# Kernel tuning notes

Hardware: AMD Instinct MI355X
Metric: run time of the kernel (lower is better)

Reference implementation:

```python
import jax, jax.numpy as jnp
import numpy as np


def conv2d(x, w, b=None, pad=0):
    # x: [N,C,H,W], w: [O,I,kh,kw] (cross-correlation, matches torch conv2d)
    out = jax.lax.conv_general_dilated(
        x, w, window_strides=(1, 1), padding=[(pad, pad), (pad, pad)],
        dimension_numbers=('NCHW', 'OIHW', 'NCHW'))
    if b is not None:
        out = out + b[None, :, None, None]
    return out


def se_block(f, w1, b1, w2, b2):
    # squeeze-excite: global avg pool -> 1x1 conv -> relu -> 1x1 conv -> sigmoid
    s = jnp.mean(f, axis=(2, 3), keepdims=True)
    s = jax.nn.relu(conv2d(s, w1, b1, pad=0))
    s = jax.nn.sigmoid(conv2d(s, w2, b2, pad=0))
    return f * s


def setup_inputs() -> dict:
    key = jax.random.key(0)
    ks = jax.random.split(key, 32)
    B, C, H, W = 8, 3, 128, 128
    F_, S, K = 128, 8, 72  # features, squeeze, n basis kernels
    rn = lambda k, shp, sc=0.05: (jax.random.normal(k, shp, dtype=jnp.float32) * sc)
    return {
        'x': jax.random.normal(ks[0], (B, C, H, W), dtype=jnp.float32),
        'w_head': rn(ks[1], (F_, C, 3, 3)), 'b_head': rn(ks[2], (F_,)),
        'w_h1a': rn(ks[3], (F_, F_, 3, 3)), 'b_h1a': rn(ks[4], (F_,)),
        'w_h1b': rn(ks[5], (F_, F_, 3, 3)), 'b_h1b': rn(ks[6], (F_,)),
        'du1_w1': rn(ks[7], (S, F_, 1, 1)), 'du1_b1': rn(ks[8], (S,)),
        'du1_w2': rn(ks[9], (F_, S, 1, 1)), 'du1_b2': rn(ks[10], (F_,)),
        'w_h2a': rn(ks[11], (F_, F_, 3, 3)), 'b_h2a': rn(ks[12], (F_,)),
        'w_h2b': rn(ks[13], (F_, F_, 3, 3)), 'b_h2b': rn(ks[14], (F_,)),
        'du2_w1': rn(ks[15], (S, F_, 1, 1)), 'du2_b1': rn(ks[16], (S,)),
        'du2_w2': rn(ks[17], (F_, S, 1, 1)), 'du2_b2': rn(ks[18], (F_,)),
        'w_tail': rn(ks[19], (K, F_, 3, 3)), 'b_tail': rn(ks[20], (K,)),
        'kernel': rn(ks[21], (K, 1, 5, 5), 0.2),  # fixed 72x5x5 basis
    }


def reference(x, w_head, b_head, w_h1a, b_h1a, w_h1b, b_h1b,
              du1_w1, du1_b1, du1_w2, du1_b2,
              w_h2a, b_h2a, w_h2b, b_h2b,
              du2_w1, du2_b1, du2_w2, du2_b2,
              w_tail, b_tail, kernel):
    B, C, H, W = x.shape
    K = kernel.shape[0]
    # trunk: head -> (conv relu)x2 -> SE -> (conv relu)x2 -> SE -> tail
    f = conv2d(x, w_head, b_head, pad=1)
    f = jax.nn.relu(conv2d(f, w_h1a, b_h1a, pad=1))
    f = jax.nn.relu(conv2d(f, w_h1b, b_h1b, pad=1))
    f = se_block(f, du1_w1, du1_b1, du1_w2, du1_b2)
    f = jax.nn.relu(conv2d(f, w_h2a, b_h2a, pad=1))
    f = jax.nn.relu(conv2d(f, w_h2b, b_h2b, pad=1))
    f = se_block(f, du2_w1, du2_b1, du2_w2, du2_b2)
    wgt = conv2d(f, w_tail, b_tail, pad=1).reshape(B, 1, K, H, W)
    # dynamic filtering: apply 72 fixed 5x5 basis kernels per channel, then
    # per-pixel weighted sum over the 72 basis responses
    xp = jnp.pad(x, ((0, 0), (0, 0), (2, 2), (2, 2)), mode='reflect')
    xp = xp.reshape(B * C, 1, H + 4, W + 4)
    x_com = conv2d(xp, kernel, None, pad=0).reshape(B, C, K, H, W)
    out = jnp.sum(wgt * x_com, axis=2)  # [B,3,H,W]
    return out
```

## Files before the change

kernel.cpp:

```cpp
#include <hip/hip_runtime.h>
#include <math.h>


typedef __attribute__((ext_vector_type(8))) short bf16x8;
typedef __attribute__((ext_vector_type(4))) float f32x4;

__device__ inline float bf2f(unsigned short u) {
    unsigned v = ((unsigned)u) << 16;
    return __builtin_bit_cast(float, v);
}
__device__ inline unsigned short f2bf(float f) {
    unsigned u = __builtin_bit_cast(unsigned, f);
    u += 0x7FFF + ((u >> 16) & 1);
    return (unsigned short)(u >> 16);
}

__global__ __launch_bounds__(256) void head_conv(
    const float* __restrict__ x, const float* __restrict__ w,
    const float* __restrict__ bias, unsigned short* __restrict__ out)
{
    __shared__ float wlds[216];
    __shared__ float tile[3][34 * 34];
    const int tid = threadIdx.x, cog = blockIdx.y, b = blockIdx.z;
    const int tile_y = (blockIdx.x >> 2) * 32, tile_x = (blockIdx.x & 3) * 32;

    if (tid < 216) {
        int co = tid & 7, rest = tid >> 3, tap = rest % 9, ci = rest / 9;
        wlds[tid] = w[((cog * 8 + co) * 3 + ci) * 9 + tap];
    }
    for (int idx = tid; idx < 3 * 34 * 34; idx += 256) {
        int ci = idx / 1156, rem = idx - ci * 1156;
        int r = rem / 34, c = rem - r * 34;
        int gy = tile_y - 1 + r, gx = tile_x - 1 + c;
        float v = 0.f;
        if ((unsigned)gy < 128u && (unsigned)gx < 128u)
            v = x[(((size_t)(b * 3 + ci)) << 14) + (gy << 7) + gx];
        tile[ci][rem] = v;
    }
    __syncthreads();

    const int ty = tid >> 4, tx = tid & 15, py = ty * 2;
    float acc[2][2][8];
    #pragma unroll
    for (int r = 0; r < 2; ++r)
        #pragma unroll
        for (int h = 0; h < 2; ++h)
            #pragma unroll
            for (int co = 0; co < 8; ++co) acc[r][h][co] = 0.f;

    #pragma unroll
    for (int ci = 0; ci < 3; ++ci) {
        #pragma unroll
        for (int ky = 0; ky < 3; ++ky) {
            #pragma unroll
            for (int kx = 0; kx < 3; ++kx) {
                const float* wp = wlds + (ci * 9 + ky * 3 + kx) * 8;
                float i00 = tile[ci][(py + ky) * 34 + tx + kx];
                float i01 = tile[ci][(py + ky) * 34 + tx + 16 + kx];
                float i10 = tile[ci][(py + 1 + ky) * 34 + tx + kx];
                float i11 = tile[ci][(py + 1 + ky) * 34 + tx + 16 + kx];
                #pragma unroll
                for (int co = 0; co < 8; ++co) {
                    float wv = wp[co];
                    acc[0][0][co] += i00 * wv;
                    acc[0][1][co] += i01 * wv;
                    acc[1][0][co] += i10 * wv;
                    acc[1][1][co] += i11 * wv;
                }
            }
        }
    }

    #pragma unroll
    for (int r = 0; r < 2; ++r) {
        #pragma unroll
        for (int h = 0; h < 2; ++h) {
            int gy = tile_y + py + r, gx = tile_x + tx + h * 16;
            bf16x8 pv;
            #pragma unroll
            for (int co = 0; co < 8; ++co)
                pv[co] = (short)f2bf(acc[r][h][co] + bias[cog * 8 + co]);
            *(bf16x8*)(out + (((((size_t)b << 14) + gy * 128 + gx)) << 7) + cog * 8) = pv;
        }
    }
}

template <int LM, int NTW, int WNSPLIT, int DOMEAN, int TAILFUSE>
__global__ __launch_bounds__(256, 2) void conv_mfma(
    const unsigned short* __restrict__ in, const unsigned short* __restrict__ wT,
    size_t wstride, const float* __restrict__ bias, unsigned short* __restrict__ out,
    float* __restrict__ meanb, const float* __restrict__ x,
    const unsigned short* __restrict__ kb, float* __restrict__ outf,
    int Coutp, int Cout, int relu)
{
    __shared__ unsigned short lds[TAILFUSE ? 26624 : 20736];
    const int tid = threadIdx.x;
    const int b = blockIdx.y;
    const int row0 = (blockIdx.x >> 3) << 4;
    const int col0 = (blockIdx.x & 7) << 4;
    const int l = tid & 63, wv = tid >> 6;
    const int li = l & 15, lq = l >> 4;
    const int m_base = WNSPLIT ? (wv >> 1) * LM : wv * LM;
    const int n_base = WNSPLIT ? (wv & 1) * NTW : 0;
    const size_t inb = ((size_t)b) << 14;
    const unsigned short* wbase = wT + (size_t)b * wstride;

    f32x4 acc[LM][NTW];
    #pragma unroll
    for (int lm = 0; lm < LM; ++lm)
        #pragma unroll
        for (int nt = 0; nt < NTW; ++nt)
            acc[lm][nt] = (f32x4){0.f, 0.f, 0.f, 0.f};

    #pragma unroll 1
    for (int half = 0; half < 2; ++half) {
        __syncthreads();
        for (int u = tid; u < 2592; u += 256) {
            int px = u >> 3, g = u & 7;
            int hr = px / 18, hc = px - hr * 18;
            int gy = row0 - 1 + hr, gx = col0 - 1 + hc;
            bf16x8 v = {0, 0, 0, 0, 0, 0, 0, 0};
            if ((unsigned)gy < 128u && (unsigned)gx < 128u)
                v = *(const bf16x8*)(in + ((inb + (gy << 7) + gx) << 7) + half * 64 + g * 8);
            int p = g ^ (px & 7);
            *(bf16x8*)(lds + px * 64 + p * 8) = v;
        }
        __syncthreads();

        auto loadB = [&](bf16x8 (&dst)[NTW], int s) {
            int tap = s >> 1, kcl = s & 1;
            const unsigned short* p = wbase +
                (size_t)(tap * 4 + half * 2 + kcl) * (Coutp * 32) +
                (n_base * 16 + li) * 32 + lq * 8;
            #pragma unroll
            for (int nt = 0; nt < NTW; ++nt)
                dst[nt] = *(const bf16x8*)(p + nt * 512);
        };
        auto compute = [&](bf16x8 (&bf)[NTW], int s) {
            int tap = s >> 1, kcl = s & 1;
            int ky = tap / 3, kx = tap - ky * 3;
            int g = kcl * 4 + lq;
            #pragma unroll
            for (int lm = 0; lm < LM; ++lm) {
                int px = (m_base + lm + ky) * 18 + li + kx;
                bf16x8 af = *(const bf16x8*)(lds + px * 64 + ((g ^ (px & 7)) * 8));
                #pragma unroll
                for (int nt = 0; nt < NTW; ++nt)
                    acc[lm][nt] = __builtin_amdgcn_mfma_f32_16x16x32_bf16(
                        af, bf[nt], acc[lm][nt], 0, 0, 0);
            }
        };

        bf16x8 bufA[NTW], bufB[NTW];
        loadB(bufA, 0);
        #pragma unroll 1
        for (int it = 0; it < 18; it += 2) {
            loadB(bufB, it + 1);
            compute(bufA, it);
            if (it + 2 < 18) loadB(bufA, it + 2);
            compute(bufB, it + 1);
        }
    }

    float bv[NTW], msum[NTW];
    #pragma unroll
    for (int nt = 0; nt < NTW; ++nt) {
        int co = (n_base + nt) * 16 + li;
        bv[nt] = (co < Cout) ? bias[co] : 0.f;
        msum[nt] = 0.f;
    }

    if (TAILFUSE) {
        __syncthreads();
        #pragma unroll
        for (int lm = 0; lm < LM; ++lm) {
            int rowl = m_base + lm;
            #pragma unroll
            for (int r = 0; r < 4; ++r) {
                int coll = lq * 4 + r;
                #pragma unroll
                for (int nt = 0; nt < NTW; ++nt)
                    lds[(rowl * 16 + coll) * 104 + nt * 16 + li] =
                        f2bf(acc[lm][nt][r] + bv[nt]);
            }
        }
        {
            bf16x8 z = {0, 0, 0, 0, 0, 0, 0, 0};
            *(bf16x8*)(lds + tid * 104 + 80) = z;
            *(bf16x8*)(lds + tid * 104 + 88) = z;
        }
        __syncthreads();

        f32x4 eacc[4][2];
        #pragma unroll
        for (int mm = 0; mm < 4; ++mm)
            #pragma unroll
            for (int nt = 0; nt < 2; ++nt)
                eacc[mm][nt] = (f32x4){0.f, 0.f, 0.f, 0.f};
        #pragma unroll
        for (int s = 0; s < 3; ++s) {
            bf16x8 kbf[2];
            #pragma unroll
            for (int nt = 0; nt < 2; ++nt)
                kbf[nt] = *(const bf16x8*)(kb + ((s * 2 + nt) * 16 + li) * 32 + lq * 8);
            #pragma unroll
            for (int mm = 0; mm < 4; ++mm) {
                int px = (wv * 4 + mm) * 16 + li;
                bf16x8 pf = *(const bf16x8*)(lds + px * 104 + s * 32 + lq * 8);
                #pragma unroll
                for (int nt = 0; nt < 2; ++nt)
                    eacc[mm][nt] = __builtin_amdgcn_mfma_f32_16x16x32_bf16(
                        pf, kbf[nt], eacc[mm][nt], 0, 0, 0);
            }
        }
        __syncthreads();

        float* elds = (float*)lds;
        #pragma unroll
        for (int mm = 0; mm < 4; ++mm) {
            #pragma unroll
            for (int nt = 0; nt < 2; ++nt) {
                int i = nt * 16 + li;
                if (i < 25) {
                    #pragma unroll
                    for (int r = 0; r < 4; ++r) {
                        int px = (wv * 4 + mm) * 16 + lq * 4 + r;
                        elds[px * 33 + i] = eacc[mm][nt][r];
                    }
                }
            }
        }
        __syncthreads();

        const int h = row0 + (tid >> 4), w = col0 + (tid & 15);
        const int pix = h * 128 + w;
        float e[25];
        #pragma unroll
        for (int i = 0; i < 25; ++i) e[i] = elds[tid * 33 + i];

        int yy[5], xx[5];
        #pragma unroll
        for (int d = 0; d < 5; ++d) {
            int y = h - 2 + d;
            yy[d] = y < 0 ? -y : (y > 127 ? 254 - y : y);
            int xv = w - 2 + d;
            xx[d] = xv < 0 ? -xv : (xv > 127 ? 254 - xv : xv);
        }
        #pragma unroll
        for (int c = 0; c < 3; ++c) {
            const float* xc = x + ((size_t)(b * 3 + c) << 14);
            float s = 0.f;
            #pragma unroll
            for (int dy = 0; dy < 5; ++dy)
                #pragma unroll
                for (int dx = 0; dx < 5; ++dx)
                    s += e[dy * 5 + dx] * xc[yy[dy] * 128 + xx[dx]];
            outf[((size_t)(b * 3 + c) << 14) + pix] = s;
        }
        return;
    }

    #pragma unroll
    for (int lm = 0; lm < LM; ++lm) {
        int row = row0 + m_base + lm;
        #pragma unroll
        for (int r = 0; r < 4; ++r) {
            int col = col0 + lq * 4 + r;
            size_t pbase = (inb + row * 128 + col) * (size_t)Coutp;
            #pragma unroll
            for (int nt = 0; nt < NTW; ++nt) {
                float v = acc[lm][nt][r] + bv[nt];
                if (relu) v = fmaxf(v, 0.f);
                if (DOMEAN) msum[nt] += v;
                out[pbase + (n_base + nt) * 16 + li] = f2bf(v);
            }
        }
    }
    if (DOMEAN) {
        #pragma unroll
        for (int nt = 0; nt < NTW; ++nt) {
            float t = msum[nt];
            t += __shfl_xor(t, 16, 64);
            t += __shfl_xor(t, 32, 64);
            if (lq == 0)
                atomicAdd(&meanb[b * 128 + (n_base + nt) * 16 + li], t);
        }
    }
}

__device__ inline void wtrans_one(const float* w, unsigned short* wT,
                                  int Co, int Coutp, int idx)
{
    int ch = idx & 31;
    int rest = idx >> 5;
    int co = rest % Coutp;
    int slice = rest / Coutp;
    int kc = slice & 3, tap = slice >> 2;
    float v = (co < Co) ? w[((size_t)(co * 128 + kc * 32 + ch)) * 9 + tap] : 0.f;
    wT[idx] = f2bf(v);
}

__global__ __launch_bounds__(256) void wtrans6(
    const float* __restrict__ w0, const float* __restrict__ w1,
    const float* __restrict__ w2, const float* __restrict__ w3,
    const float* __restrict__ w4, const float* __restrict__ kern,
    unsigned short* __restrict__ t0, unsigned short* __restrict__ t1,
    unsigned short* __restrict__ t2, unsigned short* __restrict__ t3,
    unsigned short* __restrict__ t4, unsigned short* __restrict__ kb,
    float* __restrict__ meanz)
{
    int idx = blockIdx.x * 256 + threadIdx.x;
    int y = blockIdx.y;
    if (y < 4) {
        const float* w = y == 0 ? w0 : y == 1 ? w1 : y == 2 ? w2 : w3;
        unsigned short* t = y == 0 ? t0 : y == 1 ? t1 : y == 2 ? t2 : t3;
        wtrans_one(w, t, 128, 128, idx);
    } else if (y == 4) {
        if (idx < 9 * 4 * 80 * 32) wtrans_one(w4, t4, 72, 80, idx);
    } else {
        if (idx < 3072) {
            int lq = (idx & 31) >> 3, j = idx & 7;
            int row = idx >> 5;
            int li = row & 15, snt = row >> 4;
            int s = snt >> 1, nt = snt & 1;
            int co = s * 32 + lq * 8 + j, i = nt * 16 + li;
            float v = (co < 72 && i < 25) ? kern[co * 25 + i] : 0.f;
            kb[idx] = f2bf(v);
        }
        if (idx < 2048) meanz[idx] = 0.f;
    }
}

__global__ __launch_bounds__(256) void wscale8f(
    const unsigned short* __restrict__ wT, const float* __restrict__ meanb,
    const float* __restrict__ w1, const float* __restrict__ b1,
    const float* __restrict__ w2, const float* __restrict__ b2,
    unsigned short* __restrict__ out, int Coutp)
{
    const int b = blockIdx.y, c = threadIdx.x;
    __shared__ float h1[8];
    __shared__ float sl[128];
    if (c < 8) {
        float s = 0.f;
        for (int j = 0; j < 128; ++j) s += w1[c * 128 + j] * meanb[b * 128 + j];
        h1[c] = fmaxf(s * (1.f / 16384.f) + b1[c], 0.f);
    }
    __syncthreads();
    if (c < 128) {
        float s = b2[c];
        #pragma unroll
        for (int j = 0; j < 8; ++j) s += w2[c * 8 + j] * h1[j];
        sl[c] = 1.f / (1.f + expf(-s));
    }
    __syncthreads();
    int r = blockIdx.x * 256 + c;
    int ch = r & 31;
    int kc = ((r >> 5) / Coutp) & 3;
    out[(size_t)b * (9 * 4 * Coutp * 32) + r] = f2bf(bf2f(wT[r]) * sl[kc * 32 + ch]);
}

extern "C" void kernel_launch(void* const* d_in, const int* in_sizes, int n_in,
                              void* d_out, int out_size, void* d_ws, size_t ws_size,
                              hipStream_t stream)
{
    const float* x      = (const float*)d_in[0];
    const float* w_head = (const float*)d_in[1];
    const float* b_head = (const float*)d_in[2];
    const float* w_h1a  = (const float*)d_in[3];
    const float* b_h1a  = (const float*)d_in[4];
    const float* w_h1b  = (const float*)d_in[5];
    const float* b_h1b  = (const float*)d_in[6];
    const float* du1_w1 = (const float*)d_in[7];
    const float* du1_b1 = (const float*)d_in[8];
    const float* du1_w2 = (const float*)d_in[9];
    const float* du1_b2 = (const float*)d_in[10];
    const float* w_h2a  = (const float*)d_in[11];
    const float* b_h2a  = (const float*)d_in[12];
    const float* w_h2b  = (const float*)d_in[13];
    const float* b_h2b  = (const float*)d_in[14];
    const float* du2_w1 = (const float*)d_in[15];
    const float* du2_b1 = (const float*)d_in[16];
    const float* du2_w2 = (const float*)d_in[17];
    const float* du2_b2 = (const float*)d_in[18];
    const float* w_tail = (const float*)d_in[19];
    const float* b_tail = (const float*)d_in[20];
    const float* kern   = (const float*)d_in[21];
    float* out = (float*)d_out;

    unsigned short* fb0  = (unsigned short*)d_ws;
    unsigned short* fb1  = fb0 + 16777216;
    unsigned short* wt1  = fb1 + 16777216;
    unsigned short* wt2  = wt1 + 147456;
    unsigned short* wt3  = wt2 + 147456;
    unsigned short* wt4  = wt3 + 147456;
    unsigned short* wtt  = wt4 + 147456;
    unsigned short* wsa  = wtt + 92160;
    unsigned short* wst  = wsa + 8 * 147456;
    unsigned short* kbb  = wst + 8 * 92160;
    float* mean1  = (float*)(kbb + 3072);
    float* mean2  = mean1 + 1024;

    dim3 blk(256);
    wtrans6<<<dim3(576, 6), blk, 0, stream>>>(w_h1a, w_h1b, w_h2a, w_h2b, w_tail,
                                              kern, wt1, wt2, wt3, wt4, wtt, kbb,
                                              mean1);

    head_conv<<<dim3(16, 16, 8), blk, 0, stream>>>(x, w_head, b_head, fb0);

    dim3 cgrid(64, 8);
    conv_mfma<8, 4, 1, 0, 0><<<cgrid, blk, 0, stream>>>(
        fb0, wt1, 0, b_h1a, fb1, nullptr, nullptr, nullptr, nullptr, 128, 128, 1);
    conv_mfma<8, 4, 1, 1, 0><<<cgrid, blk, 0, stream>>>(
        fb1, wt2, 0, b_h1b, fb0, mean1, nullptr, nullptr, nullptr, 128, 128, 1);

    wscale8f<<<dim3(576, 8), blk, 0, stream>>>(wt3, mean1, du1_w1, du1_b1,
                                               du1_w2, du1_b2, wsa, 128);

    conv_mfma<8, 4, 1, 0, 0><<<cgrid, blk, 0, stream>>>(
        fb0, wsa, 147456, b_h2a, fb1, nullptr, nullptr, nullptr, nullptr, 128, 128, 1);
    conv_mfma<8, 4, 1, 1, 0><<<cgrid, blk, 0, stream>>>(
        fb1, wt4, 0, b_h2b, fb0, mean2, nullptr, nullptr, nullptr, 128, 128, 1);

    wscale8f<<<dim3(360, 8), blk, 0, stream>>>(wtt, mean2, du2_w1, du2_b1,
                                               du2_w2, du2_b2, wst, 80);

    conv_mfma<4, 5, 0, 0, 1><<<cgrid, blk, 0, stream>>>(
        fb0, wst, 92160, b_tail, nullptr, nullptr, x, kbb, out, 80, 72, 0);
}
```

Measured before the change: 335.0 us.

## Prefetch second input-channel half into registers during first-half MFMA compute

The 3x3 conv kernel loaded both 64-channel halves of the input halo tile into LDS sequentially, stalling on global loads before each half. It now issues the global loads for the second half into 11 registers per thread while the first half's MFMA loop runs, then writes them to LDS after a barrier. This hides global-load latency behind compute, but adds about 44 VGPRs per thread, which may lower occupancy or cause spills.

```diff
diff --git a/kernel.cpp b/kernel.cpp
--- a/kernel.cpp
+++ b/kernel.cpp
@@ -112,54 +112,90 @@
         for (int nt = 0; nt < NTW; ++nt)
             acc[lm][nt] = (f32x4){0.f, 0.f, 0.f, 0.f};
 
-    #pragma unroll 1
-    for (int half = 0; half < 2; ++half) {
-        __syncthreads();
-        for (int u = tid; u < 2592; u += 256) {
+    auto loadB = [&](int half, bf16x8 (&dst)[NTW], int s) {
+        int tap = s >> 1, kcl = s & 1;
+        const unsigned short* p = wbase +
+            (size_t)(tap * 4 + half * 2 + kcl) * (Coutp * 32) +
+            (n_base * 16 + li) * 32 + lq * 8;
+        #pragma unroll
+        for (int nt = 0; nt < NTW; ++nt)
+            dst[nt] = *(const bf16x8*)(p + nt * 512);
+    };
+    auto compute = [&](bf16x8 (&bf)[NTW], int s) {
+        int tap = s >> 1, kcl = s & 1;
+        int ky = tap / 3, kx = tap - ky * 3;
+        int g = kcl * 4 + lq;
+        #pragma unroll
+        for (int lm = 0; lm < LM; ++lm) {
+            int px = (m_base + lm + ky) * 18 + li + kx;
+            bf16x8 af = *(const bf16x8*)(lds + px * 64 + ((g ^ (px & 7)) * 8));
+            #pragma unroll
+            for (int nt = 0; nt < NTW; ++nt)
+                acc[lm][nt] = __builtin_amdgcn_mfma_f32_16x16x32_bf16(
+                    af, bf[nt], acc[lm][nt], 0, 0, 0);
+        }
+    };
+
+    #pragma unroll
+    for (int k = 0; k < 11; ++k) {
+        int u = tid + (k << 8);
+        if (u < 2592) {
             int px = u >> 3, g = u & 7;
             int hr = px / 18, hc = px - hr * 18;
             int gy = row0 - 1 + hr, gx = col0 - 1 + hc;
             bf16x8 v = {0, 0, 0, 0, 0, 0, 0, 0};
             if ((unsigned)gy < 128u && (unsigned)gx < 128u)
-                v = *(const bf16x8*)(in + ((inb + (gy << 7) + gx) << 7) + half * 64 + g * 8);
-            int p = g ^ (px & 7);
-            *(bf16x8*)(lds + px * 64 + p * 8) = v;
-        }
-        __syncthreads();
-
-        auto loadB = [&](bf16x8 (&dst)[NTW], int s) {
-            int tap = s >> 1, kcl = s & 1;
-            const unsigned short* p = wbase +
-                (size_t)(tap * 4 + half * 2 + kcl) * (Coutp * 32) +
-                (n_base * 16 + li) * 32 + lq * 8;
-            #pragma unroll
-            for (int nt = 0; nt < NTW; ++nt)
-                dst[nt] = *(const bf16x8*)(p + nt * 512);
-        };
-        auto compute = [&](bf16x8 (&bf)[NTW], int s) {
-            int tap = s >> 1, kcl = s & 1;
-            int ky = tap / 3, kx = tap - ky * 3;
-            int g = kcl * 4 + lq;
-            #pragma unroll
-            for (int lm = 0; lm < LM; ++lm) {
-                int px = (m_base + lm + ky) * 18 + li + kx;
-                bf16x8 af = *(const bf16x8*)(lds + px * 64 + ((g ^ (px & 7)) * 8));
-                #pragma unroll
-                for (int nt = 0; nt < NTW; ++nt)
-                    acc[lm][nt] = __builtin_amdgcn_mfma_f32_16x16x32_bf16(
-                        af, bf[nt], acc[lm][nt], 0, 0, 0);
-            }
-        };
-
-        bf16x8 bufA[NTW], bufB[NTW];
-        loadB(bufA, 0);
-        #pragma unroll 1
-        for (int it = 0; it < 18; it += 2) {
-            loadB(bufB, it + 1);
-            compute(bufA, it);
-            if (it + 2 < 18) loadB(bufA, it + 2);
-            compute(bufB, it + 1);
-        }
+                v = *(const bf16x8*)(in + ((inb + (gy << 7) + gx) << 7) + g * 8);
+            *(bf16x8*)(lds + px * 64 + ((g ^ (px & 7)) * 8)) = v;
+        }
+    }
+    __syncthreads();
+
+    bf16x8 bufA[NTW], bufB[NTW];
+    bf16x8 sreg[11];
+    loadB(0, bufA, 0);
+    loadB(0, bufB, 1);
+    #pragma unroll
+    for (int k = 0; k < 11; ++k) {
+        int u = tid + (k << 8);
+        sreg[k] = (bf16x8){0, 0, 0, 0, 0, 0, 0, 0};
+        if (u < 2592) {
+            int px = u >> 3, g = u & 7;
+            int hr = px / 18, hc = px - hr * 18;
+            int gy = row0 - 1 + hr, gx = col0 - 1 + hc;
+            if ((unsigned)gy < 128u && (unsigned)gx < 128u)
+                sreg[k] = *(const bf16x8*)(in + ((inb + (gy << 7) + gx) << 7) + 64 + g * 8);
+        }
+    }
+    compute(bufA, 0);
+    loadB(0, bufA, 2);
+    compute(bufB, 1);
+    #pragma unroll 1
+    for (int it = 2; it < 18; it += 2) {
+        loadB(0, bufB, it + 1);
+        compute(bufA, it);
+        if (it + 2 < 18) loadB(0, bufA, it + 2);
+        compute(bufB, it + 1);
+    }
+
+    __syncthreads();
+    #pragma unroll
+    for (int k = 0; k < 11; ++k) {
+        int u = tid + (k << 8);
+        if (u < 2592) {
+            int px = u >> 3, g = u & 7;
+            *(bf16x8*)(lds + px * 64 + ((g ^ (px & 7)) * 8)) = sreg[k];
+        }
+    }
+    __syncthreads();
+
+    loadB(1, bufA, 0);
+    #pragma unroll 1
+    for (int it = 0; it < 18; it += 2) {
+        loadB(1, bufB, it + 1);
+        compute(bufA, it);
+        if (it + 2 < 18) loadB(1, bufA, it + 2);
+        compute(bufB, it + 1);
     }
 
     float bv[NTW], msum[NTW];
```

Result: slower. 343.4 us (+2.5%).

## Double-buffer input halo in quarters via direct global-to-LDS async loads

Applied to the files above, without the earlier changes.

Replaces the two-half synchronous register-staged LDS fill with four 32-channel quarters loaded directly into LDS using global_load_lds, double-buffered so the next quarter's halo load overlaps MFMA compute on the current one. Out-of-bounds pixels read from a zeroed workspace buffer instead of branching to a zero store, and precomputed per-thread source offsets replace the per-iteration division. This removes the exposed load-then-sync bubble per half at the cost of more barriers, a new swizzle scheme, and reliance on the zero buffer being cleared by the setup kernel.

```diff
diff --git a/kernel.cpp b/kernel.cpp
--- a/kernel.cpp
+++ b/kernel.cpp
@@ -91,7 +91,7 @@
     size_t wstride, const float* __restrict__ bias, unsigned short* __restrict__ out,
     float* __restrict__ meanb, const float* __restrict__ x,
     const unsigned short* __restrict__ kb, float* __restrict__ outf,
-    int Coutp, int Cout, int relu)
+    const unsigned short* __restrict__ zbuf, int Coutp, int Cout, int relu)
 {
     __shared__ unsigned short lds[TAILFUSE ? 26624 : 20736];
     const int tid = threadIdx.x;
@@ -102,7 +102,7 @@
     const int li = l & 15, lq = l >> 4;
     const int m_base = WNSPLIT ? (wv >> 1) * LM : wv * LM;
     const int n_base = WNSPLIT ? (wv & 1) * NTW : 0;
-    const size_t inb = ((size_t)b) << 14;
+    const unsigned short* inb7 = in + ((size_t)b << 21);
     const unsigned short* wbase = wT + (size_t)b * wstride;
 
     f32x4 acc[LM][NTW];
@@ -112,54 +112,79 @@
         for (int nt = 0; nt < NTW; ++nt)
             acc[lm][nt] = (f32x4){0.f, 0.f, 0.f, 0.f};
 
-    #pragma unroll 1
-    for (int half = 0; half < 2; ++half) {
-        __syncthreads();
-        for (int u = tid; u < 2592; u += 256) {
-            int px = u >> 3, g = u & 7;
-            int hr = px / 18, hc = px - hr * 18;
-            int gy = row0 - 1 + hr, gx = col0 - 1 + hc;
-            bf16x8 v = {0, 0, 0, 0, 0, 0, 0, 0};
-            if ((unsigned)gy < 128u && (unsigned)gx < 128u)
-                v = *(const bf16x8*)(in + ((inb + (gy << 7) + gx) << 7) + half * 64 + g * 8);
-            int p = g ^ (px & 7);
-            *(bf16x8*)(lds + px * 64 + p * 8) = v;
-        }
-        __syncthreads();
-
-        auto loadB = [&](bf16x8 (&dst)[NTW], int s) {
-            int tap = s >> 1, kcl = s & 1;
-            const unsigned short* p = wbase +
-                (size_t)(tap * 4 + half * 2 + kcl) * (Coutp * 32) +
-                (n_base * 16 + li) * 32 + lq * 8;
+    int soff[6];
+    #pragma unroll
+    for (int i = 0; i < 6; ++i) {
+        int base = (i < 5) ? (i * 4 + wv) * 64 : 1232;
+        int u = base + l;
+        int px = u >> 2, p = u & 3;
+        int g = p ^ (px & 3);
+        int hr = px / 18, hc = px - hr * 18;
+        int gy = row0 - 1 + hr, gx = col0 - 1 + hc;
+        soff[i] = ((unsigned)gy < 128u && (unsigned)gx < 128u)
+                      ? ((((gy << 7) + gx) << 7) + g * 8) : -1;
+    }
+
+    auto stageQ = [&](int q) {
+        unsigned short* dbuf = lds + (q & 1) * 10368;
+        const int qo = q * 32;
+        #pragma unroll
+        for (int i = 0; i < 6; ++i) {
+            if (i == 5 && wv != 0) continue;
+            int base = (i < 5) ? (i * 4 + wv) * 64 : 1232;
+            const unsigned short* src =
+                (soff[i] >= 0) ? (inb7 + soff[i] + qo) : zbuf;
+            __builtin_amdgcn_global_load_lds((const void*)src,
+                                             (void*)(dbuf + base * 8), 16, 0, 0);
+        }
+    };
+    auto loadB = [&](int q, bf16x8 (&dst)[NTW], int tap) {
+        const unsigned short* p = wbase +
+            (size_t)(tap * 4 + q) * (Coutp * 32) +
+            (n_base * 16 + li) * 32 + lq * 8;
+        #pragma unroll
+        for (int nt = 0; nt < NTW; ++nt)
+            dst[nt] = *(const bf16x8*)(p + nt * 512);
+    };
+    auto compute = [&](const unsigned short* lbuf, bf16x8 (&bf)[NTW], int tap) {
+        int ky = tap / 3, kx = tap - ky * 3;
+        #pragma unroll
+        for (int lm = 0; lm < LM; ++lm) {
+            int px = (m_base + lm + ky) * 18 + li + kx;
+            bf16x8 af = *(const bf16x8*)(lbuf + px * 32 + ((lq ^ (px & 3)) * 8));
             #pragma unroll
             for (int nt = 0; nt < NTW; ++nt)
-                dst[nt] = *(const bf16x8*)(p + nt * 512);
-        };
-        auto compute = [&](bf16x8 (&bf)[NTW], int s) {
-            int tap = s >> 1, kcl = s & 1;
-            int ky = tap / 3, kx = tap - ky * 3;
-            int g = kcl * 4 + lq;
-            #pragma unroll
-            for (int lm = 0; lm < LM; ++lm) {
-                int px = (m_base + lm + ky) * 18 + li + kx;
-                bf16x8 af = *(const bf16x8*)(lds + px * 64 + ((g ^ (px & 7)) * 8));
-                #pragma unroll
-                for (int nt = 0; nt < NTW; ++nt)
-                    acc[lm][nt] = __builtin_amdgcn_mfma_f32_16x16x32_bf16(
-                        af, bf[nt], acc[lm][nt], 0, 0, 0);
-            }
-        };
-
-        bf16x8 bufA[NTW], bufB[NTW];
-        loadB(bufA, 0);
-        #pragma unroll 1
-        for (int it = 0; it < 18; it += 2) {
-            loadB(bufB, it + 1);
-            compute(bufA, it);
-            if (it + 2 < 18) loadB(bufA, it + 2);
-            compute(bufB, it + 1);
-        }
+                acc[lm][nt] = __builtin_amdgcn_mfma_f32_16x16x32_bf16(
+                    af, bf[nt], acc[lm][nt], 0, 0, 0);
+        }
+    };
+
+    stageQ(0);
+    __syncthreads();
+    #pragma unroll
+    for (int q = 0; q < 4; ++q) {
+        const unsigned short* lbuf = lds + (q & 1) * 10368;
+        bf16x8 bA[NTW], bB[NTW];
+        loadB(q, bA, 0);
+        loadB(q, bB, 1);
+        if (q < 3) stageQ(q + 1);
+        compute(lbuf, bA, 0);
+        loadB(q, bA, 2);
+        compute(lbuf, bB, 1);
+        loadB(q, bB, 3);
+        compute(lbuf, bA, 2);
+        loadB(q, bA, 4);
+        compute(lbuf, bB, 3);
+        loadB(q, bB, 5);
+        compute(lbuf, bA, 4);
+        loadB(q, bA, 6);
+        compute(lbuf, bB, 5);
+        loadB(q, bB, 7);
+        compute(lbuf, bA, 6);
+        loadB(q, bA, 8);
+        compute(lbuf, bB, 7);
+        compute(lbuf, bA, 8);
+        if (q < 3) __syncthreads();
     }
 
     float bv[NTW], msum[NTW];
@@ -266,7 +291,7 @@
         #pragma unroll
         for (int r = 0; r < 4; ++r) {
             int col = col0 + lq * 4 + r;
-            size_t pbase = (inb + row * 128 + col) * (size_t)Coutp;
+            size_t pbase = ((((size_t)b << 14) + row * 128 + col)) * (size_t)Coutp;
             #pragma unroll
             for (int nt = 0; nt < NTW; ++nt) {
                 float v = acc[lm][nt][r] + bv[nt];
@@ -327,7 +352,7 @@
             float v = (co < 72 && i < 25) ? kern[co * 25 + i] : 0.f;
             kb[idx] = f2bf(v);
         }
-        if (idx < 2048) meanz[idx] = 0.f;
+        if (idx < 2112) meanz[idx] = 0.f;
     }
 }
 
@@ -399,6 +424,7 @@
     unsigned short* kbb  = wst + 8 * 92160;
     float* mean1  = (float*)(kbb + 3072);
     float* mean2  = mean1 + 1024;
+    unsigned short* zbuf = (unsigned short*)(mean2 + 1024);
 
     dim3 blk(256);
     wtrans6<<<dim3(576, 6), blk, 0, stream>>>(w_h1a, w_h1b, w_h2a, w_h2b, w_tail,
@@ -409,21 +435,21 @@
 
     dim3 cgrid(64, 8);
     conv_mfma<8, 4, 1, 0, 0><<<cgrid, blk, 0, stream>>>(
-        fb0, wt1, 0, b_h1a, fb1, nullptr, nullptr, nullptr, nullptr, 128, 128, 1);
+        fb0, wt1, 0, b_h1a, fb1, nullptr, nullptr, nullptr, nullptr, zbuf, 128, 128, 1);
     conv_mfma<8, 4, 1, 1, 0><<<cgrid, blk, 0, stream>>>(
-        fb1, wt2, 0, b_h1b, fb0, mean1, nullptr, nullptr, nullptr, 128, 128, 1);
+        fb1, wt2, 0, b_h1b, fb0, mean1, nullptr, nullptr, nullptr, zbuf, 128, 128, 1);
 
     wscale8f<<<dim3(576, 8), blk, 0, stream>>>(wt3, mean1, du1_w1, du1_b1,
                                                du1_w2, du1_b2, wsa, 128);
 
     conv_mfma<8, 4, 1, 0, 0><<<cgrid, blk, 0, stream>>>(
-        fb0, wsa, 147456, b_h2a, fb1, nullptr, nullptr, nullptr, nullptr, 128, 128, 1);
+        fb0, wsa, 147456, b_h2a, fb1, nullptr, nullptr, nullptr, nullptr, zbuf, 128, 128, 1);
     conv_mfma<8, 4, 1, 1, 0><<<cgrid, blk, 0, stream>>>(
-        fb1, wt4, 0, b_h2b, fb0, mean2, nullptr, nullptr, nullptr, 128, 128, 1);
+        fb1, wt4, 0, b_h2b, fb0, mean2, nullptr, nullptr, nullptr, zbuf, 128, 128, 1);
 
     wscale8f<<<dim3(360, 8), blk, 0, stream>>>(wtt, mean2, du2_w1, du2_b1,
                                                du2_w2, du2_b2, wst, 80);
 
     conv_mfma<4, 5, 0, 0, 1><<<cgrid, blk, 0, stream>>>(
-        fb0, wst, 92160, b_tail, nullptr, nullptr, x, kbb, out, 80, 72, 0);
-}
+        fb0, wst, 92160, b_tail, nullptr, nullptr, x, kbb, out, zbuf, 80, 72, 0);
+}
```

Result: slower. 369.2 us (+10.2%).

## Fuse SE scaling into consumer convs and merge head conv with weight prep

Applied to the files above, without the earlier changes.

Removes the two wscale8f kernels that wrote per-batch scaled weight copies. Instead, each consuming conv computes the squeeze-excite scale from the accumulated means into LDS and, judging by the SCALEA template flag, applies it to the input activations it loads. It also merges the head conv and weight transposition into one prep kernel, cutting two launches and the per-batch weight traffic. In exchange, every conv block recomputes the small SE MLP and does an extra multiply on its staged activations.

```diff
diff --git a/kernel.cpp b/kernel.cpp
--- a/kernel.cpp
+++ b/kernel.cpp
@@ -13,279 +13,6 @@
     unsigned u = __builtin_bit_cast(unsigned, f);
     u += 0x7FFF + ((u >> 16) & 1);
     return (unsigned short)(u >> 16);
-}
-
-__global__ __launch_bounds__(256) void head_conv(
-    const float* __restrict__ x, const float* __restrict__ w,
-    const float* __restrict__ bias, unsigned short* __restrict__ out)
-{
-    __shared__ float wlds[216];
-    __shared__ float tile[3][34 * 34];
-    const int tid = threadIdx.x, cog = blockIdx.y, b = blockIdx.z;
-    const int tile_y = (blockIdx.x >> 2) * 32, tile_x = (blockIdx.x & 3) * 32;
-
-    if (tid < 216) {
-        int co = tid & 7, rest = tid >> 3, tap = rest % 9, ci = rest / 9;
-        wlds[tid] = w[((cog * 8 + co) * 3 + ci) * 9 + tap];
-    }
-    for (int idx = tid; idx < 3 * 34 * 34; idx += 256) {
-        int ci = idx / 1156, rem = idx - ci * 1156;
-        int r = rem / 34, c = rem - r * 34;
-        int gy = tile_y - 1 + r, gx = tile_x - 1 + c;
-        float v = 0.f;
-        if ((unsigned)gy < 128u && (unsigned)gx < 128u)
-            v = x[(((size_t)(b * 3 + ci)) << 14) + (gy << 7) + gx];
-        tile[ci][rem] = v;
-    }
-    __syncthreads();
-
-    const int ty = tid >> 4, tx = tid & 15, py = ty * 2;
-    float acc[2][2][8];
-    #pragma unroll
-    for (int r = 0; r < 2; ++r)
-        #pragma unroll
-        for (int h = 0; h < 2; ++h)
-            #pragma unroll
-            for (int co = 0; co < 8; ++co) acc[r][h][co] = 0.f;
-
-    #pragma unroll
-    for (int ci = 0; ci < 3; ++ci) {
-        #pragma unroll
-        for (int ky = 0; ky < 3; ++ky) {
-            #pragma unroll
-            for (int kx = 0; kx < 3; ++kx) {
-                const float* wp = wlds + (ci * 9 + ky * 3 + kx) * 8;
-                float i00 = tile[ci][(py + ky) * 34 + tx + kx];
-                float i01 = tile[ci][(py + ky) * 34 + tx + 16 + kx];
-                float i10 = tile[ci][(py + 1 + ky) * 34 + tx + kx];
-                float i11 = tile[ci][(py + 1 + ky) * 34 + tx + 16 + kx];
-                #pragma unroll
-                for (int co = 0; co < 8; ++co) {
-                    float wv = wp[co];
-                    acc[0][0][co] += i00 * wv;
-                    acc[0][1][co] += i01 * wv;
-                    acc[1][0][co] += i10 * wv;
-                    acc[1][1][co] += i11 * wv;
-                }
-            }
-        }
-    }
-
-    #pragma unroll
-    for (int r = 0; r < 2; ++r) {
-        #pragma unroll
-        for (int h = 0; h < 2; ++h) {
-            int gy = tile_y + py + r, gx = tile_x + tx + h * 16;
-            bf16x8 pv;
-            #pragma unroll
-            for (int co = 0; co < 8; ++co)
-                pv[co] = (short)f2bf(acc[r][h][co] + bias[cog * 8 + co]);
-            *(bf16x8*)(out + (((((size_t)b << 14) + gy * 128 + gx)) << 7) + cog * 8) = pv;
-        }
-    }
-}
-
-template <int LM, int NTW, int WNSPLIT, int DOMEAN, int TAILFUSE>
-__global__ __launch_bounds__(256, 2) void conv_mfma(
-    const unsigned short* __restrict__ in, const unsigned short* __restrict__ wT,
-    size_t wstride, const float* __restrict__ bias, unsigned short* __restrict__ out,
-    float* __restrict__ meanb, const float* __restrict__ x,
-    const unsigned short* __restrict__ kb, float* __restrict__ outf,
-    int Coutp, int Cout, int relu)
-{
-    __shared__ unsigned short lds[TAILFUSE ? 26624 : 20736];
-    const int tid = threadIdx.x;
-    const int b = blockIdx.y;
-    const int row0 = (blockIdx.x >> 3) << 4;
-    const int col0 = (blockIdx.x & 7) << 4;
-    const int l = tid & 63, wv = tid >> 6;
-    const int li = l & 15, lq = l >> 4;
-    const int m_base = WNSPLIT ? (wv >> 1) * LM : wv * LM;
-    const int n_base = WNSPLIT ? (wv & 1) * NTW : 0;
-    const size_t inb = ((size_t)b) << 14;
-    const unsigned short* wbase = wT + (size_t)b * wstride;
-
-    f32x4 acc[LM][NTW];
-    #pragma unroll
-    for (int lm = 0; lm < LM; ++lm)
-        #pragma unroll
-        for (int nt = 0; nt < NTW; ++nt)
-            acc[lm][nt] = (f32x4){0.f, 0.f, 0.f, 0.f};
-
-    #pragma unroll 1
-    for (int half = 0; half < 2; ++half) {
-        __syncthreads();
-        for (int u = tid; u < 2592; u += 256) {
-            int px = u >> 3, g = u & 7;
-            int hr = px / 18, hc = px - hr * 18;
-            int gy = row0 - 1 + hr, gx = col0 - 1 + hc;
-            bf16x8 v = {0, 0, 0, 0, 0, 0, 0, 0};
-            if ((unsigned)gy < 128u && (unsigned)gx < 128u)
-                v = *(const bf16x8*)(in + ((inb + (gy << 7) + gx) << 7) + half * 64 + g * 8);
-            int p = g ^ (px & 7);
-            *(bf16x8*)(lds + px * 64 + p * 8) = v;
-        }
-        __syncthreads();
-
-        auto loadB = [&](bf16x8 (&dst)[NTW], int s) {
-            int tap = s >> 1, kcl = s & 1;
-            const unsigned short* p = wbase +
-                (size_t)(tap * 4 + half * 2 + kcl) * (Coutp * 32) +
-                (n_base * 16 + li) * 32 + lq * 8;
-            #pragma unroll
-            for (int nt = 0; nt < NTW; ++nt)
-                dst[nt] = *(const bf16x8*)(p + nt * 512);
-        };
-        auto compute = [&](bf16x8 (&bf)[NTW], int s) {
-            int tap = s >> 1, kcl = s & 1;
-            int ky = tap / 3, kx = tap - ky * 3;
-            int g = kcl * 4 + lq;
-            #pragma unroll
-            for (int lm = 0; lm < LM; ++lm) {
-                int px = (m_base + lm + ky) * 18 + li + kx;
-                bf16x8 af = *(const bf16x8*)(lds + px * 64 + ((g ^ (px & 7)) * 8));
-                #pragma unroll
-                for (int nt = 0; nt < NTW; ++nt)
-                    acc[lm][nt] = __builtin_amdgcn_mfma_f32_16x16x32_bf16(
-                        af, bf[nt], acc[lm][nt], 0, 0, 0);
-            }
-        };
-
-        bf16x8 bufA[NTW], bufB[NTW];
-        loadB(bufA, 0);
-        #pragma unroll 1
-        for (int it = 0; it < 18; it += 2) {
-            loadB(bufB, it + 1);
-            compute(bufA, it);
-            if (it + 2 < 18) loadB(bufA, it + 2);
-            compute(bufB, it + 1);
-        }
-    }
-
-    float bv[NTW], msum[NTW];
-    #pragma unroll
-    for (int nt = 0; nt < NTW; ++nt) {
-        int co = (n_base + nt) * 16 + li;
-        bv[nt] = (co < Cout) ? bias[co] : 0.f;
-        msum[nt] = 0.f;
-    }
-
-    if (TAILFUSE) {
-        __syncthreads();
-        #pragma unroll
-        for (int lm = 0; lm < LM; ++lm) {
-            int rowl = m_base + lm;
-            #pragma unroll
-            for (int r = 0; r < 4; ++r) {
-                int coll = lq * 4 + r;
-                #pragma unroll
-                for (int nt = 0; nt < NTW; ++nt)
-                    lds[(rowl * 16 + coll) * 104 + nt * 16 + li] =
-                        f2bf(acc[lm][nt][r] + bv[nt]);
-            }
-        }
-        {
-            bf16x8 z = {0, 0, 0, 0, 0, 0, 0, 0};
-            *(bf16x8*)(lds + tid * 104 + 80) = z;
-            *(bf16x8*)(lds + tid * 104 + 88) = z;
-        }
-        __syncthreads();
-
-        f32x4 eacc[4][2];
-        #pragma unroll
-        for (int mm = 0; mm < 4; ++mm)
-            #pragma unroll
-            for (int nt = 0; nt < 2; ++nt)
-                eacc[mm][nt] = (f32x4){0.f, 0.f, 0.f, 0.f};
-        #pragma unroll
-        for (int s = 0; s < 3; ++s) {
-            bf16x8 kbf[2];
-            #pragma unroll
-            for (int nt = 0; nt < 2; ++nt)
-                kbf[nt] = *(const bf16x8*)(kb + ((s * 2 + nt) * 16 + li) * 32 + lq * 8);
-            #pragma unroll
-            for (int mm = 0; mm < 4; ++mm) {
-                int px = (wv * 4 + mm) * 16 + li;
-                bf16x8 pf = *(const bf16x8*)(lds + px * 104 + s * 32 + lq * 8);
-                #pragma unroll
-                for (int nt = 0; nt < 2; ++nt)
-                    eacc[mm][nt] = __builtin_amdgcn_mfma_f32_16x16x32_bf16(
-                        pf, kbf[nt], eacc[mm][nt], 0, 0, 0);
-            }
-        }
-        __syncthreads();
-
-        float* elds = (float*)lds;
-        #pragma unroll
-        for (int mm = 0; mm < 4; ++mm) {
-            #pragma unroll
-            for (int nt = 0; nt < 2; ++nt) {
-                int i = nt * 16 + li;
-                if (i < 25) {
-                    #pragma unroll
-                    for (int r = 0; r < 4; ++r) {
-                        int px = (wv * 4 + mm) * 16 + lq * 4 + r;
-                        elds[px * 33 + i] = eacc[mm][nt][r];
-                    }
-                }
-            }
-        }
-        __syncthreads();
-
-        const int h = row0 + (tid >> 4), w = col0 + (tid & 15);
-        const int pix = h * 128 + w;
-        float e[25];
-        #pragma unroll
-        for (int i = 0; i < 25; ++i) e[i] = elds[tid * 33 + i];
-
-        int yy[5], xx[5];
-        #pragma unroll
-        for (int d = 0; d < 5; ++d) {
-            int y = h - 2 + d;
-            yy[d] = y < 0 ? -y : (y > 127 ? 254 - y : y);
-            int xv = w - 2 + d;
-            xx[d] = xv < 0 ? -xv : (xv > 127 ? 254 - xv : xv);
-        }
-        #pragma unroll
-        for (int c = 0; c < 3; ++c) {
-            const float* xc = x + ((size_t)(b * 3 + c) << 14);
-            float s = 0.f;
-            #pragma unroll
-            for (int dy = 0; dy < 5; ++dy)
-                #pragma unroll
-                for (int dx = 0; dx < 5; ++dx)
-                    s += e[dy * 5 + dx] * xc[yy[dy] * 128 + xx[dx]];
-            outf[((size_t)(b * 3 + c) << 14) + pix] = s;
-        }
-        return;
-    }
-
-    #pragma unroll
-    for (int lm = 0; lm < LM; ++lm) {
-        int row = row0 + m_base + lm;
-        #pragma unroll
-        for (int r = 0; r < 4; ++r) {
-            int col = col0 + lq * 4 + r;
-            size_t pbase = (inb + row * 128 + col) * (size_t)Coutp;
-            #pragma unroll
-            for (int nt = 0; nt < NTW; ++nt) {
-                float v = acc[lm][nt][r] + bv[nt];
-                if (relu) v = fmaxf(v, 0.f);
-                if (DOMEAN) msum[nt] += v;
-                out[pbase + (n_base + nt) * 16 + li] = f2bf(v);
-            }
-        }
-    }
-    if (DOMEAN) {
-        #pragma unroll
-        for (int nt = 0; nt < NTW; ++nt) {
-            float t = msum[nt];
-            t += __shfl_xor(t, 16, 64);
-            t += __shfl_xor(t, 32, 64);
-            if (lq == 0)
-                atomicAdd(&meanb[b * 128 + (n_base + nt) * 16 + li], t);
-        }
-    }
 }
 
 __device__ inline void wtrans_one(const float* w, unsigned short* wT,
@@ -300,7 +27,9 @@
     wT[idx] = f2bf(v);
 }
 
-__global__ __launch_bounds__(256) void wtrans6(
+__global__ __launch_bounds__(256) void prep(
+    const float* __restrict__ x, const float* __restrict__ wh,
+    const float* __restrict__ bh, unsigned short* __restrict__ fb0,
     const float* __restrict__ w0, const float* __restrict__ w1,
     const float* __restrict__ w2, const float* __restrict__ w3,
     const float* __restrict__ w4, const float* __restrict__ kern,
@@ -309,54 +38,332 @@
     unsigned short* __restrict__ t4, unsigned short* __restrict__ kb,
     float* __restrict__ meanz)
 {
-    int idx = blockIdx.x * 256 + threadIdx.x;
-    int y = blockIdx.y;
-    if (y < 4) {
-        const float* w = y == 0 ? w0 : y == 1 ? w1 : y == 2 ? w2 : w3;
-        unsigned short* t = y == 0 ? t0 : y == 1 ? t1 : y == 2 ? t2 : t3;
-        wtrans_one(w, t, 128, 128, idx);
-    } else if (y == 4) {
-        if (idx < 9 * 4 * 80 * 32) wtrans_one(w4, t4, 72, 80, idx);
-    } else {
-        if (idx < 3072) {
-            int lq = (idx & 31) >> 3, j = idx & 7;
-            int row = idx >> 5;
-            int li = row & 15, snt = row >> 4;
-            int s = snt >> 1, nt = snt & 1;
-            int co = s * 32 + lq * 8 + j, i = nt * 16 + li;
-            float v = (co < 72 && i < 25) ? kern[co * 25 + i] : 0.f;
-            kb[idx] = f2bf(v);
-        }
-        if (idx < 2048) meanz[idx] = 0.f;
-    }
-}
-
-__global__ __launch_bounds__(256) void wscale8f(
-    const unsigned short* __restrict__ wT, const float* __restrict__ meanb,
-    const float* __restrict__ w1, const float* __restrict__ b1,
-    const float* __restrict__ w2, const float* __restrict__ b2,
-    unsigned short* __restrict__ out, int Coutp)
+    __shared__ float wlds[216];
+    __shared__ float tile[3][34 * 34];
+    const int tid = threadIdx.x;
+    const int bid = blockIdx.x;
+
+    if (bid >= 2048) {
+        int r = bid - 2048;
+        int y = r / 576;
+        int idx = (r - y * 576) * 256 + tid;
+        if (y < 4) {
+            const float* w = y == 0 ? w0 : y == 1 ? w1 : y == 2 ? w2 : w3;
+            unsigned short* t = y == 0 ? t0 : y == 1 ? t1 : y == 2 ? t2 : t3;
+            wtrans_one(w, t, 128, 128, idx);
+        } else if (y == 4) {
+            if (idx < 9 * 4 * 80 * 32) wtrans_one(w4, t4, 72, 80, idx);
+        } else {
+            if (idx < 3072) {
+                int lq = (idx & 31) >> 3, j = idx & 7;
+                int row = idx >> 5;
+                int li = row & 15, snt = row >> 4;
+                int s = snt >> 1, nt = snt & 1;
+                int co = s * 32 + lq * 8 + j, i = nt * 16 + li;
+                float v = (co < 72 && i < 25) ? kern[co * 25 + i] : 0.f;
+                kb[idx] = f2bf(v);
+            }
+            if (idx < 2048) meanz[idx] = 0.f;
+        }
+        return;
+    }
+
+    const int bx = bid & 15, cog = (bid >> 4) & 15, b = bid >> 8;
+    const int tile_y = (bx >> 2) * 32, tile_x = (bx & 3) * 32;
+
+    if (tid < 216) {
+        int co = tid & 7, rest = tid >> 3, tap = rest % 9, ci = rest / 9;
+        wlds[tid] = wh[((cog * 8 + co) * 3 + ci) * 9 + tap];
+    }
+    for (int idx = tid; idx < 3 * 34 * 34; idx += 256) {
+        int ci = idx / 1156, rem = idx - ci * 1156;
+        int rr = rem / 34, c = rem - rr * 34;
+        int gy = tile_y - 1 + rr, gx = tile_x - 1 + c;
+        float v = 0.f;
+        if ((unsigned)gy < 128u && (unsigned)gx < 128u)
+            v = x[(((size_t)(b * 3 + ci)) << 14) + (gy << 7) + gx];
+        tile[ci][rem] = v;
+    }
+    __syncthreads();
+
+    const int ty = tid >> 4, tx = tid & 15, py = ty * 2;
+    float acc[2][2][8];
+    #pragma unroll
+    for (int r = 0; r < 2; ++r)
+        #pragma unroll
+        for (int h = 0; h < 2; ++h)
+            #pragma unroll
+            for (int co = 0; co < 8; ++co) acc[r][h][co] = 0.f;
+
+    #pragma unroll
+    for (int ci = 0; ci < 3; ++ci) {
+        #pragma unroll
+        for (int ky = 0; ky < 3; ++ky) {
+            #pragma unroll
+            for (int kx = 0; kx < 3; ++kx) {
+                const float* wp = wlds + (ci * 9 + ky * 3 + kx) * 8;
+                float i00 = tile[ci][(py + ky) * 34 + tx + kx];
+                float i01 = tile[ci][(py + ky) * 34 + tx + 16 + kx];
+                float i10 = tile[ci][(py + 1 + ky) * 34 + tx + kx];
+                float i11 = tile[ci][(py + 1 + ky) * 34 + tx + 16 + kx];
+                #pragma unroll
+                for (int co = 0; co < 8; ++co) {
+                    float wv = wp[co];
+                    acc[0][0][co] += i00 * wv;
+                    acc[0][1][co] += i01 * wv;
+                    acc[1][0][co] += i10 * wv;
+                    acc[1][1][co] += i11 * wv;
+                }
+            }
+        }
+    }
+
+    #pragma unroll
+    for (int r = 0; r < 2; ++r) {
+        #pragma unroll
+        for (int h = 0; h < 2; ++h) {
+            int gy = tile_y + py + r, gx = tile_x + tx + h * 16;
+            bf16x8 pv;
+            #pragma unroll
+            for (int co = 0; co < 8; ++co)
+                pv[co] = (short)f2bf(acc[r][h][co] + bh[cog * 8 + co]);
+            *(bf16x8*)(fb0 + (((((size_t)b << 14) + gy * 128 + gx)) << 7) + cog * 8) = pv;
+        }
+    }
+}
+
+template <int LM, int NTW, int WNSPLIT, int DOMEAN, int TAILFUSE, int SCALEA>
+__global__ __launch_bounds__(256, 2) void conv_mfma(
+    const unsigned short* __restrict__ in, const unsigned short* __restrict__ wT,
+    const float* __restrict__ bias, unsigned short* __restrict__ out,
+    float* __restrict__ meanb, const float* __restrict__ se_mean,
+    const float* __restrict__ sw1, const float* __restrict__ sb1,
+    const float* __restrict__ sw2, const float* __restrict__ sb2,
+    const float* __restrict__ x, const unsigned short* __restrict__ kb,
+    float* __restrict__ outf, int Coutp, int Cout, int relu)
 {
-    const int b = blockIdx.y, c = threadIdx.x;
-    __shared__ float h1[8];
-    __shared__ float sl[128];
-    if (c < 8) {
-        float s = 0.f;
-        for (int j = 0; j < 128; ++j) s += w1[c * 128 + j] * meanb[b * 128 + j];
-        h1[c] = fmaxf(s * (1.f / 16384.f) + b1[c], 0.f);
-    }
-    __syncthreads();
-    if (c < 128) {
-        float s = b2[c];
-        #pragma unroll
-        for (int j = 0; j < 8; ++j) s += w2[c * 8 + j] * h1[j];
-        sl[c] = 1.f / (1.f + expf(-s));
-    }
-    __syncthreads();
-    int r = blockIdx.x * 256 + c;
-    int ch = r & 31;
-    int kc = ((r >> 5) / Coutp) & 3;
-    out[(size_t)b * (9 * 4 * Coutp * 32) + r] = f2bf(bf2f(wT[r]) * sl[kc * 32 + ch]);
+    __shared__ unsigned short lds[TAILFUSE ? 26624 : 20736];
+    __shared__ float slds[136];
+    const int tid = threadIdx.x;
+    const int b = blockIdx.y;
+    const int row0 = (blockIdx.x >> 3) << 4;
+    const int col0 = (blockIdx.x & 7) << 4;
+    const int l = tid & 63, wv = tid >> 6;
+    const int li = l & 15, lq = l >> 4;
+    const int m_base = WNSPLIT ? (wv >> 1) * LM : wv * LM;
+    const int n_base = WNSPLIT ? (wv & 1) * NTW : 0;
+    const size_t inb = ((size_t)b) << 14;
+    const unsigned short* wbase = wT;
+
+    if (SCALEA) {
+        if (tid < 8) {
+            float s = 0.f;
+            for (int j = 0; j < 128; ++j)
+                s += sw1[tid * 128 + j] * se_mean[b * 128 + j];
+            slds[128 + tid] = fmaxf(s * (1.f / 16384.f) + sb1[tid], 0.f);
+        }
+        __syncthreads();
+        if (tid < 128) {
+            float s = sb2[tid];
+            #pragma unroll
+            for (int j = 0; j < 8; ++j) s += sw2[tid * 8 + j] * slds[128 + j];
+            slds[tid] = 1.f / (1.f + expf(-s));
+        }
+        __syncthreads();
+    }
+
+    f32x4 acc[LM][NTW];
+    #pragma unroll
+    for (int lm = 0; lm < LM; ++lm)
+        #pragma unroll
+        for (int nt = 0; nt < NTW; ++nt)
+            acc[lm][nt] = (f32x4){0.f, 0.f, 0.f, 0.f};
+
+    #pragma unroll 1
+    for (int half = 0; half < 2; ++half) {
+        float msc[8];
+        if (SCALEA) {
+            #pragma unroll
+            for (int j = 0; j < 8; ++j)
+                msc[j] = slds[half * 64 + (tid & 7) * 8 + j];
+        }
+        __syncthreads();
+        for (int u = tid; u < 2592; u += 256) {
+            int px = u >> 3, g = u & 7;
+            int hr = px / 18, hc = px - hr * 18;
+            int gy = row0 - 1 + hr, gx = col0 - 1 + hc;
+            bf16x8 v = {0, 0, 0, 0, 0, 0, 0, 0};
+            if ((unsigned)gy < 128u && (unsigned)gx < 128u)
+                v = *(const bf16x8*)(in + ((inb + (gy << 7) + gx) << 7) + half * 64 + g * 8);
+            if (SCALEA) {
+                #pragma unroll
+                for (int j = 0; j < 8; ++j)
+                    v[j] = (short)f2bf(bf2f((unsigned short)v[j]) * msc[j]);
+            }
+            int p = g ^ (px & 7);
+            *(bf16x8*)(lds + px * 64 + p * 8) = v;
+        }
+        __syncthreads();
+
+        auto loadB = [&](bf16x8 (&dst)[NTW], int s) {
+            int tap = s >> 1, kcl = s & 1;
+            const unsigned short* p = wbase +
+                (size_t)(tap * 4 + half * 2 + kcl) * (Coutp * 32) +
+                (n_base * 16 + li) * 32 + lq * 8;
+            #pragma unroll
+            for (int nt = 0; nt < NTW; ++nt)
+                dst[nt] = *(const bf16x8*)(p + nt * 512);
+        };
+        auto compute = [&](bf16x8 (&bf)[NTW], int s) {
+            int tap = s >> 1, kcl = s & 1;
+            int ky = tap / 3, kx = tap - ky * 3;
+            int g = kcl * 4 + lq;
+            #pragma unroll
+            for (int lm = 0; lm < LM; ++lm) {
+                int px = (m_base + lm + ky) * 18 + li + kx;
+                bf16x8 af = *(const bf16x8*)(lds + px * 64 + ((g ^ (px & 7)) * 8));
+                #pragma unroll
+                for (int nt = 0; nt < NTW; ++nt)
+                    acc[lm][nt] = __builtin_amdgcn_mfma_f32_16x16x32_bf16(
+                        af, bf[nt], acc[lm][nt], 0, 0, 0);
+            }
+        };
+
+        bf16x8 bufA[NTW], bufB[NTW];
+        loadB(bufA, 0);
+        #pragma unroll 1
+        for (int it = 0; it < 18; it += 2) {
+            loadB(bufB, it + 1);
+            compute(bufA, it);
+            if (it + 2 < 18) loadB(bufA, it + 2);
+            compute(bufB, it + 1);
+        }
+    }
+
+    float bv[NTW], msum[NTW];
+    #pragma unroll
+    for (int nt = 0; nt < NTW; ++nt) {
+        int co = (n_base + nt) * 16 + li;
+        bv[nt] = (co < Cout) ? bias[co] : 0.f;
+        msum[nt] = 0.f;
+    }
+
+    if (TAILFUSE) {
+        __syncthreads();
+        #pragma unroll
+        for (int lm = 0; lm < LM; ++lm) {
+            int rowl = m_base + lm;
+            #pragma unroll
+            for (int r = 0; r < 4; ++r) {
+                int coll = lq * 4 + r;
+                #pragma unroll
+                for (int nt = 0; nt < NTW; ++nt)
+                    lds[(rowl * 16 + coll) * 104 + nt * 16 + li] =
+                        f2bf(acc[lm][nt][r] + bv[nt]);
+            }
+        }
+        {
+            bf16x8 z = {0, 0, 0, 0, 0, 0, 0, 0};
+            *(bf16x8*)(lds + tid * 104 + 80) = z;
+            *(bf16x8*)(lds + tid * 104 + 88) = z;
+        }
+        __syncthreads();
+
+        f32x4 eacc[4][2];
+        #pragma unroll
+        for (int mm = 0; mm < 4; ++mm)
+            #pragma unroll
+            for (int nt = 0; nt < 2; ++nt)
+                eacc[mm][nt] = (f32x4){0.f, 0.f, 0.f, 0.f};
+        #pragma unroll
+        for (int s = 0; s < 3; ++s) {
+            bf16x8 kbf[2];
+            #pragma unroll
+            for (int nt = 0; nt < 2; ++nt)
+                kbf[nt] = *(const bf16x8*)(kb + ((s * 2 + nt) * 16 + li) * 32 + lq * 8);
+            #pragma unroll
+            for (int mm = 0; mm < 4; ++mm) {
+                int px = (wv * 4 + mm) * 16 + li;
+                bf16x8 pf = *(const bf16x8*)(lds + px * 104 + s * 32 + lq * 8);
+                #pragma unroll
+                for (int nt = 0; nt < 2; ++nt)
+                    eacc[mm][nt] = __builtin_amdgcn_mfma_f32_16x16x32_bf16(
+                        pf, kbf[nt], eacc[mm][nt], 0, 0, 0);
+            }
+        }
+        __syncthreads();
+
+        float* elds = (float*)lds;
+        #pragma unroll
+        for (int mm = 0; mm < 4; ++mm) {
+            #pragma unroll
+            for (int nt = 0; nt < 2; ++nt) {
+                int i = nt * 16 + li;
+                if (i < 25) {
+                    #pragma unroll
+                    for (int r = 0; r < 4; ++r) {
+                        int px = (wv * 4 + mm) * 16 + lq * 4 + r;
+                        elds[px * 33 + i] = eacc[mm][nt][r];
+                    }
+                }
+            }
+        }
+        __syncthreads();
+
+        const int h = row0 + (tid >> 4), w = col0 + (tid & 15);
+        const int pix = h * 128 + w;
+        float e[25];
+        #pragma unroll
+        for (int i = 0; i < 25; ++i) e[i] = elds[tid * 33 + i];
+
+        int yy[5], xx[5];
+        #pragma unroll
+        for (int d = 0; d < 5; ++d) {
+            int y = h - 2 + d;
+            yy[d] = y < 0 ? -y : (y > 127 ? 254 - y : y);
+            int xv = w - 2 + d;
+            xx[d] = xv < 0 ? -xv : (xv > 127 ? 254 - xv : xv);
+        }
+        #pragma unroll
+        for (int c = 0; c < 3; ++c) {
+            const float* xc = x + ((size_t)(b * 3 + c) << 14);
+            float s = 0.f;
+            #pragma unroll
+            for (int dy = 0; dy < 5; ++dy)
+                #pragma unroll
+                for (int dx = 0; dx < 5; ++dx)
+                    s += e[dy * 5 + dx] * xc[yy[dy] * 128 + xx[dx]];
+            outf[((size_t)(b * 3 + c) << 14) + pix] = s;
+        }
+        return;
+    }
+
+    #pragma unroll
+    for (int lm = 0; lm < LM; ++lm) {
+        int row = row0 + m_base + lm;
+        #pragma unroll
+        for (int r = 0; r < 4; ++r) {
+            int col = col0 + lq * 4 + r;
+            size_t pbase = (inb + row * 128 + col) * (size_t)Coutp;
+            #pragma unroll
+            for (int nt = 0; nt < NTW; ++nt) {
+                float v = acc[lm][nt][r] + bv[nt];
+                if (relu) v = fmaxf(v, 0.f);
+                if (DOMEAN) msum[nt] += v;
+                out[pbase + (n_base + nt) * 16 + li] = f2bf(v);
+            }
+        }
+    }
+    if (DOMEAN) {
+        #pragma unroll
+        for (int nt = 0; nt < NTW; ++nt) {
+            float t = msum[nt];
+            t += __shfl_xor(t, 16, 64);
+            t += __shfl_xor(t, 32, 64);
+            if (lq == 0)
+                atomicAdd(&meanb[b * 128 + (n_base + nt) * 16 + li], t);
+        }
+    }
 }
 
 extern "C" void kernel_launch(void* const* d_in, const int* in_sizes, int n_in,
@@ -394,36 +401,32 @@
     unsigned short* wt3  = wt2 + 147456;
     unsigned short* wt4  = wt3 + 147456;
     unsigned short* wtt  = wt4 + 147456;
-    unsigned short* wsa  = wtt + 92160;
-    unsigned short* wst  = wsa + 8 * 147456;
-    unsigned short* kbb  = wst + 8 * 92160;
+    unsigned short* kbb  = wtt + 92160;
     float* mean1  = (float*)(kbb + 3072);
     float* mean2  = mean1 + 1024;
 
     dim3 blk(256);
-    wtrans6<<<dim3(576, 6), blk, 0, stream>>>(w_h1a, w_h1b, w_h2a, w_h2b, w_tail,
-                                              kern, wt1, wt2, wt3, wt4, wtt, kbb,
-                                              mean1);
-
-    head_conv<<<dim3(16, 16, 8), blk, 0, stream>>>(x, w_head, b_head, fb0);
+    prep<<<dim3(5504), blk, 0, stream>>>(x, w_head, b_head, fb0,
+                                         w_h1a, w_h1b, w_h2a, w_h2b, w_tail,
+                                         kern, wt1, wt2, wt3, wt4, wtt, kbb,
+                                         mean1);
 
     dim3 cgrid(64, 8);
-    conv_mfma<8, 4, 1, 0, 0><<<cgrid, blk, 0, stream>>>(
-        fb0, wt1, 0, b_h1a, fb1, nullptr, nullptr, nullptr, nullptr, 128, 128, 1);
-    conv_mfma<8, 4, 1, 1, 0><<<cgrid, blk, 0, stream>>>(
-        fb1, wt2, 0, b_h1b, fb0, mean1, nullptr, nullptr, nullptr, 128, 128, 1);
-
-    wscale8f<<<dim3(576, 8), blk, 0, stream>>>(wt3, mean1, du1_w1, du1_b1,
-                                               du1_w2, du1_b2, wsa, 128);
-
-    conv_mfma<8, 4, 1, 0, 0><<<cgrid, blk, 0, stream>>>(
-        fb0, wsa, 147456, b_h2a, fb1, nullptr, nullptr, nullptr, nullptr, 128, 128, 1);
-    conv_mfma<8, 4, 1, 1, 0><<<cgrid, blk, 0, stream>>>(
-        fb1, wt4, 0, b_h2b, fb0, mean2, nullptr, nullptr, nullptr, 128, 128, 1);
-
-    wscale8f<<<dim3(360, 8), blk, 0, stream>>>(wtt, mean2, du2_w1, du2_b1,
-                                               du2_w2, du2_b2, wst, 80);
-
-    conv_mfma<4, 5, 0, 0, 1><<<cgrid, blk, 0, stream>>>(
-        fb0, wst, 92160, b_tail, nullptr, nullptr, x, kbb, out, 80, 72, 0);
-}
+    conv_mfma<8, 4, 1, 0, 0, 0><<<cgrid, blk, 0, stream>>>(
+        fb0, wt1, b_h1a, fb1, nullptr, nullptr, nullptr, nullptr, nullptr,
+        nullptr, nullptr, nullptr, nullptr, 128, 128, 1);
+    conv_mfma<8, 4, 1, 1, 0, 0><<<cgrid, blk, 0, stream>>>(
+        fb1, wt2, b_h1b, fb0, mean1, nullptr, nullptr, nullptr, nullptr,
+        nullptr, nullptr, nullptr, nullptr, 128, 128, 1);
+
+    conv_mfma<8, 4, 1, 0, 0, 1><<<cgrid, blk, 0, stream>>>(
+        fb0, wt3, b_h2a, fb1, nullptr, mean1, du1_w1, du1_b1, du1_w2, du1_b2,
+        nullptr, nullptr, nullptr, 128, 128, 1);
+    conv_mfma<8, 4, 1, 1, 0, 0><<<cgrid, blk, 0, stream>>>(
+        fb1, wt4, b_h2b, fb0, mean2, nullptr, nullptr, nullptr, nullptr,
+        nullptr, nullptr, nullptr, nullptr, 128, 128, 1);
+
+    conv_mfma<4, 5, 0, 0, 1, 1><<<cgrid, blk, 0, stream>>>(
+        fb0, wtt, b_tail, nullptr, nullptr, mean2, du2_w1, du2_b1, du2_w2,
+        du2_b2, x, kbb, out, 80, 72, 0);
+}
```

New measurement: 331.7 us. Within noise of the previous version (-1.0%).
